# Kernel tuning notes

Measured on AMD Instinct MI355X. Metric: run time of the kernel, lower is better.

Reference implementation:

```python
import jax, jax.numpy as jnp
import numpy as np

B, S, D, H, T_OUT = 256, 256, 64, 1024, 32  # batch, enc seq, input dim, hidden, decode steps


def setup_inputs() -> dict:
    key = jax.random.key(0)
    ks = jax.random.split(key, 15)
    p = lambda k, shape: jax.random.normal(k, shape, jnp.float32) * 0.05
    return {
        "X": jax.random.normal(ks[0], (B, S, D), jnp.float32),
        # encoder LSTM (2 layers); bias = b_ih + b_hh fused (same math)
        "enc_Wih0": p(ks[1], (4 * H, D)), "enc_Whh0": p(ks[2], (4 * H, H)), "enc_b0": p(ks[3], (4 * H,)),
        "enc_Wih1": p(ks[4], (4 * H, H)), "enc_Whh1": p(ks[5], (4 * H, H)), "enc_b1": p(ks[6], (4 * H,)),
        # decoder LSTM (2 layers, scalar input)
        "dec_Wih0": p(ks[7], (4 * H, 1)), "dec_Whh0": p(ks[8], (4 * H, H)), "dec_b0": p(ks[9], (4 * H,)),
        "dec_Wih1": p(ks[10], (4 * H, H)), "dec_Whh1": p(ks[11], (4 * H, H)), "dec_b1": p(ks[12], (4 * H,)),
        # output projection hidden -> 1
        "fc_W": p(ks[13], (1, H)), "fc_b": p(ks[14], (1,)),
    }


def _cell(x, h, c, Wih, Whh, b):
    # torch LSTM cell, gate order i, f, g, o
    gates = x @ Wih.T + h @ Whh.T + b  # [B, 4H]
    i, f, g, o = jnp.split(gates, 4, axis=-1)
    c = jax.nn.sigmoid(f) * c + jax.nn.sigmoid(i) * jnp.tanh(g)
    h = jax.nn.sigmoid(o) * jnp.tanh(c)
    return h, c


def reference(X, enc_Wih0, enc_Whh0, enc_b0, enc_Wih1, enc_Whh1, enc_b1,
              dec_Wih0, dec_Whh0, dec_b0, dec_Wih1, dec_Whh1, dec_b1,
              fc_W, fc_b):
    batch = X.shape[0]
    zeros = jnp.zeros((batch, H), X.dtype)

    def enc_layer(Wih, Whh, b, xs):  # xs: [S, B, Din]
        def step(carry, x_t):
            h, c = carry
            h, c = _cell(x_t, h, c, Wih, Whh, b)
            return (h, c), h
        (h, c), hs = jax.lax.scan(step, (zeros, zeros), xs)
        return hs, h, c

    xs = jnp.swapaxes(X, 0, 1)  # time-major [S, B, D]
    hs0, h0, c0 = enc_layer(enc_Wih0, enc_Whh0, enc_b0, xs)
    _, h1, c1 = enc_layer(enc_Wih1, enc_Whh1, enc_b1, hs0)

    inp0 = jnp.zeros((batch, 1), X.dtype)

    def dec_step(carry, _):
        dh0, dc0, dh1, dc1, inp = carry
        dh0, dc0 = _cell(inp, dh0, dc0, dec_Wih0, dec_Whh0, dec_b0)
        dh1, dc1 = _cell(dh0, dh1, dc1, dec_Wih1, dec_Whh1, dec_b1)
        pred = dh1 @ fc_W.T + fc_b  # [B, 1]; dropout is identity at inference
        return (dh0, dc0, dh1, dc1, pred), pred

    _, preds = jax.lax.scan(dec_step, (h0, c0, h1, c1, inp0), None, length=T_OUT)
    return jnp.transpose(preds, (1, 0, 2))  # [B, T_OUT, 1]
```

## Files before the change

### kernel.cpp

```cpp
#include <hip/hip_runtime.h>

#define B_ 256
#define S_ 256
#define D_ 64
#define H_ 1024
#define G4 4096
#define TOUT 32

typedef unsigned short u16;
typedef __attribute__((ext_vector_type(8))) short short8;
typedef __attribute__((ext_vector_type(4))) float float4v;

__device__ __forceinline__ float bf2f(u16 b) {
  return __uint_as_float(((unsigned int)b) << 16);
}
__device__ __forceinline__ u16 f2bf(float f) {
  unsigned int u = __float_as_uint(f);
  unsigned int r = (u + 0x7fffu + ((u >> 16) & 1u)) >> 16;
  return (u16)r;
}
__device__ __forceinline__ unsigned pack2(float a, float b) {
  return (unsigned)f2bf(a) | ((unsigned)f2bf(b) << 16);
}
__device__ __forceinline__ float sigm(float x) {
  return 1.f / (1.f + __expf(-x));
}
__device__ __forceinline__ float tanh_(float x) {
  float xc = fminf(fmaxf(x, -15.f), 15.f);
  float e = __expf(2.f * xc);
  return (e - 1.f) / (e + 1.f);
}

__global__ __launch_bounds__(256) void cvt_kernel(const float* __restrict__ src,
                                                  u16* __restrict__ dst, int n) {
  for (int i = blockIdx.x * blockDim.x + threadIdx.x; i < n;
       i += gridDim.x * blockDim.x)
    dst[i] = f2bf(src[i]);
}

__global__ __launch_bounds__(256) void zero_kernel(uint4* __restrict__ p, int n16) {
  for (int i = blockIdx.x * blockDim.x + threadIdx.x; i < n16;
       i += gridDim.x * blockDim.x)
    p[i] = make_uint4(0u, 0u, 0u, 0u);
}

struct LayerDesc {
  const u16* A0; int lda0;
  const u16* A1; int lda1; int klen0;
  const void* W0; int ldw0;
  const void* W1; int ldw1; int Ktot;
  const float* bias;
  const float* wcol;
  const float* inp;
  float* c;
  u16* h;
  int active;
  float* gout;
  const float* fcW;
  float* pred;
};

template <bool WF32>
__global__ __launch_bounds__(256) void lstm_step_kernel(LayerDesc dA, LayerDesc dB)
{
  const bool second = (blockIdx.y >= 4);
  const LayerDesc d = second ? dB : dA;
  if (!d.active) return;

  __shared__ u16 As[2][64][72];
  __shared__ u16 Bs[2][64][72];
  __shared__ float Gs[64][68];

  const int tid = threadIdx.x;
  const int m0 = (second ? (blockIdx.y - 4) : blockIdx.y) * 64;
  const int n0 = blockIdx.x * 64;
  const int ub = n0 >> 2;
  const int r = tid >> 2;
  const int q = tid & 3;
  const int lane = tid & 63;
  const int wv = tid >> 6;
  const int wm = (wv >> 1) * 32;
  const int wn = (wv & 1) * 32;
  const int l16 = lane & 15;
  const int quad = lane >> 4;

  const int klen0 = d.klen0;
  const u16* aw0 = d.A0 + (size_t)(m0 + r) * d.lda0;
  const u16* aw1 = d.A1 + (size_t)(m0 + r) * d.lda1;
  const int orow = (r & 3) * H_ + ub + (r >> 2);
  const u16* bw0_h = (const u16*)d.W0 + (size_t)orow * d.ldw0;
  const u16* bw1_h = (const u16*)d.W1 + (size_t)orow * d.ldw1;
  const float* bw0_f = (const float*)d.W0 + (size_t)orow * d.ldw0;
  const float* bw1_f = (const float*)d.W1 + (size_t)orow * d.ldw1;

  uint4 av0, av1, bv0, bv1;
  float4 bf0, bf1, bf2, bf3;

  auto load_chunk = [&](int kc) {
    const int kg = kc * 64 + q * 16;
    const bool first = kg < klen0;
    const u16* pa = first ? (aw0 + kg) : (aw1 + (kg - klen0));
    av0 = *(const uint4*)pa;
    av1 = *(const uint4*)(pa + 8);
    if constexpr (WF32) {
      const float* pb = first ? (bw0_f + kg) : (bw1_f + (kg - klen0));
      bf0 = *(const float4*)pb;
      bf1 = *(const float4*)(pb + 4);
      bf2 = *(const float4*)(pb + 8);
      bf3 = *(const float4*)(pb + 12);
    } else {
      const u16* pb = first ? (bw0_h + kg) : (bw1_h + (kg - klen0));
      bv0 = *(const uint4*)pb;
      bv1 = *(const uint4*)(pb + 8);
    }
  };

  auto stage = [&](int buf) {
    if constexpr (WF32) {
      bv0 = make_uint4(pack2(bf0.x, bf0.y), pack2(bf0.z, bf0.w),
                       pack2(bf1.x, bf1.y), pack2(bf1.z, bf1.w));
      bv1 = make_uint4(pack2(bf2.x, bf2.y), pack2(bf2.z, bf2.w),
                       pack2(bf3.x, bf3.y), pack2(bf3.z, bf3.w));
    }
    *(uint4*)&As[buf][r][q * 16]     = av0;
    *(uint4*)&As[buf][r][q * 16 + 8] = av1;
    *(uint4*)&Bs[buf][r][q * 16]     = bv0;
    *(uint4*)&Bs[buf][r][q * 16 + 8] = bv1;
  };

  float4v acc00 = {}, acc01 = {}, acc10 = {}, acc11 = {};
  const int nch = d.Ktot >> 6;

  load_chunk(0);
  stage(0);
  if (nch > 1) load_chunk(1);
  __syncthreads();

  for (int kc = 0; kc < nch; ++kc) {
    const int cur = kc & 1;
#pragma unroll
    for (int ks = 0; ks < 2; ++ks) {
      const int kb = ks * 32 + quad * 8;
      short8 a0 = *(const short8*)&As[cur][wm + l16][kb];
      short8 a1 = *(const short8*)&As[cur][wm + 16 + l16][kb];
      short8 b0 = *(const short8*)&Bs[cur][wn + l16][kb];
      short8 b1 = *(const short8*)&Bs[cur][wn + 16 + l16][kb];
      acc00 = __builtin_amdgcn_mfma_f32_16x16x32_bf16(a0, b0, acc00, 0, 0, 0);
      acc01 = __builtin_amdgcn_mfma_f32_16x16x32_bf16(a0, b1, acc01, 0, 0, 0);
      acc10 = __builtin_amdgcn_mfma_f32_16x16x32_bf16(a1, b0, acc10, 0, 0, 0);
      acc11 = __builtin_amdgcn_mfma_f32_16x16x32_bf16(a1, b1, acc11, 0, 0, 0);
    }
    if (kc + 1 < nch) {
      stage(cur ^ 1);
      if (kc + 2 < nch) load_chunk(kc + 2);
      __syncthreads();
    }
  }

#pragma unroll
  for (int rr = 0; rr < 4; ++rr) {
    Gs[wm + quad * 4 + rr][wn + l16]           = acc00[rr];
    Gs[wm + quad * 4 + rr][wn + 16 + l16]      = acc01[rr];
    Gs[wm + 16 + quad * 4 + rr][wn + l16]      = acc10[rr];
    Gs[wm + 16 + quad * 4 + rr][wn + 16 + l16] = acc11[rr];
  }
  __syncthreads();

  if (d.gout != nullptr) {
#pragma unroll
    for (int it = 0; it < 4; ++it) {
      const int p = tid + it * 256;
      const int bl = p >> 4;
      const int u = p & 15;
      const int J = ub + u;
      const int bg = m0 + bl;
      const float4v g = *(const float4v*)&Gs[bl][u * 4];
      *(float4*)&d.gout[((size_t)bg * H_ + J) * 4] =
          make_float4(g[0], g[1], g[2], g[3]);
    }
    return;
  }

#pragma unroll
  for (int it = 0; it < 4; ++it) {
    const int p = tid + it * 256;
    const int bl = p >> 4;
    const int u = p & 15;
    const int J = ub + u;
    const int bg = m0 + bl;
    const float4v g = *(const float4v*)&Gs[bl][u * 4];
    float pi = g[0] + d.bias[J];
    float pf = g[1] + d.bias[H_ + J];
    float pg = g[2] + d.bias[2 * H_ + J];
    float po = g[3] + d.bias[3 * H_ + J];
    if (d.inp != nullptr) {
      const float iv = d.inp[bg];
      pi += iv * d.wcol[J];
      pf += iv * d.wcol[H_ + J];
      pg += iv * d.wcol[2 * H_ + J];
      po += iv * d.wcol[3 * H_ + J];
    }
    const size_t idx = (size_t)bg * H_ + J;
    const float c = d.c[idx];
    const float cn = sigm(pf) * c + sigm(pi) * tanh_(pg);
    d.c[idx] = cn;
    const float hv = sigm(po) * tanh_(cn);
    d.h[idx] = f2bf(hv);
    if (d.pred != nullptr) {
      float s = hv * d.fcW[J];
      s += __shfl_xor(s, 1, 64);
      s += __shfl_xor(s, 2, 64);
      s += __shfl_xor(s, 4, 64);
      s += __shfl_xor(s, 8, 64);
      if (u == 0) atomicAdd(&d.pred[bg], s);
    }
  }
}

__global__ __launch_bounds__(256) void dec_cell_kernel(
    const float* __restrict__ GBUF, const float* __restrict__ bias,
    const float* __restrict__ wcol, const float* __restrict__ pred_prev,
    const float* __restrict__ fcb, float* __restrict__ C,
    u16* __restrict__ hout)
{
  const int b = blockIdx.x;
  const int tid = threadIdx.x;
  const float iv = (pred_prev != nullptr) ? (pred_prev[b] + fcb[0]) : 0.f;
#pragma unroll
  for (int k = 0; k < 4; ++k) {
    const int J = tid + k * 256;
    const float4 g = *(const float4*)&GBUF[((size_t)b * H_ + J) * 4];
    const float pi = g.x + bias[J]          + iv * wcol[J];
    const float pf = g.y + bias[H_ + J]     + iv * wcol[H_ + J];
    const float pg = g.z + bias[2 * H_ + J] + iv * wcol[2 * H_ + J];
    const float po = g.w + bias[3 * H_ + J] + iv * wcol[3 * H_ + J];
    const size_t idx = (size_t)b * H_ + J;
    const float c0 = C[idx];
    const float cn = sigm(pf) * c0 + sigm(pi) * tanh_(pg);
    C[idx] = cn;
    hout[idx] = f2bf(sigm(po) * tanh_(cn));
  }
}

__global__ __launch_bounds__(256) void dec_out_kernel(
    const float* __restrict__ PRED, const float* __restrict__ fcb,
    float* __restrict__ out)
{
  const int gid = blockIdx.x * 256 + threadIdx.x;
  const int b = gid >> 5;
  const int t = gid & 31;
  out[gid] = PRED[t * B_ + b] + fcb[0];
}

__global__ __launch_bounds__(256) void fc_kernel(
    const u16* __restrict__ h1, const float* __restrict__ fcW,
    const float* __restrict__ fcb, float* __restrict__ out,
    float* __restrict__ inp, int t)
{
  const int b = blockIdx.x;
  const int tid = threadIdx.x;
  const u16* hr = h1 + (size_t)b * H_ + tid * 4;
  const float* wr = fcW + tid * 4;
  float s = 0.f;
#pragma unroll
  for (int j = 0; j < 4; ++j) s += bf2f(hr[j]) * wr[j];
#pragma unroll
  for (int off = 32; off > 0; off >>= 1) s += __shfl_down(s, off, 64);
  __shared__ float red[4];
  if ((tid & 63) == 0) red[tid >> 6] = s;
  __syncthreads();
  if (tid == 0) {
    const float p = red[0] + red[1] + red[2] + red[3] + fcb[0];
    out[(size_t)b * TOUT + t] = p;
    inp[b] = p;
  }
}

extern "C" void kernel_launch(void* const* d_in, const int* in_sizes, int n_in,
                              void* d_out, int out_size, void* d_ws, size_t ws_size,
                              hipStream_t stream)
{
  const float* X     = (const float*)d_in[0];
  const float* eWih0 = (const float*)d_in[1];
  const float* eWhh0 = (const float*)d_in[2];
  const float* eb0   = (const float*)d_in[3];
  const float* eWih1 = (const float*)d_in[4];
  const float* eWhh1 = (const float*)d_in[5];
  const float* eb1   = (const float*)d_in[6];
  const float* dWih0 = (const float*)d_in[7];
  const float* dWhh0 = (const float*)d_in[8];
  const float* db0   = (const float*)d_in[9];
  const float* dWih1 = (const float*)d_in[10];
  const float* dWhh1 = (const float*)d_in[11];
  const float* db1   = (const float*)d_in[12];
  const float* fcW   = (const float*)d_in[13];
  const float* fcb   = (const float*)d_in[14];
  float* out = (float*)d_out;

  char* ws = (char*)d_ws;
  size_t off = 0;
  auto alloc = [&](size_t bytes) -> void* {
    void* p = ws + off;
    off += (bytes + 255) & ~(size_t)255;
    return p;
  };
  u16* h0buf[2], *h1buf[2];
  h0buf[0] = (u16*)alloc((size_t)B_ * H_ * 2);
  h0buf[1] = (u16*)alloc((size_t)B_ * H_ * 2);
  h1buf[0] = (u16*)alloc((size_t)B_ * H_ * 2);
  h1buf[1] = (u16*)alloc((size_t)B_ * H_ * 2);
  float* C0   = (float*)alloc((size_t)B_ * H_ * 4);
  float* C1   = (float*)alloc((size_t)B_ * H_ * 4);
  float* INP  = (float*)alloc(B_ * 4);
  float* PRED = (float*)alloc((size_t)TOUT * B_ * 4);
  const size_t zbytes = off;
  u16* XB = (u16*)alloc((size_t)B_ * S_ * D_ * 2);
  u16* WB_eWih0 = (u16*)alloc((size_t)G4 * D_ * 2);
  u16* WB_eWhh0 = (u16*)alloc((size_t)G4 * H_ * 2);
  u16* WB_eWih1 = (u16*)alloc((size_t)G4 * H_ * 2);
  u16* WB_eWhh1 = (u16*)alloc((size_t)G4 * H_ * 2);
  u16* WB_dWhh0 = (u16*)alloc((size_t)G4 * H_ * 2);
  u16* WB_dWih1 = (u16*)alloc((size_t)G4 * H_ * 2);
  u16* WB_dWhh1 = (u16*)alloc((size_t)G4 * H_ * 2);
  float* GBUF   = (float*)alloc((size_t)B_ * H_ * 4 * 4);
  const size_t need_full = off;
  const bool fast = (ws_size >= need_full);

  zero_kernel<<<dim3(256), dim3(256), 0, stream>>>((uint4*)ws, (int)(zbytes / 16));
  cvt_kernel<<<dim3(1024), dim3(256), 0, stream>>>(X, XB, B_ * S_ * D_);
  if (fast) {
    cvt_kernel<<<dim3(256), dim3(256), 0, stream>>>(eWih0, WB_eWih0, G4 * D_);
    cvt_kernel<<<dim3(1024), dim3(256), 0, stream>>>(eWhh0, WB_eWhh0, G4 * H_);
    cvt_kernel<<<dim3(1024), dim3(256), 0, stream>>>(eWih1, WB_eWih1, G4 * H_);
    cvt_kernel<<<dim3(1024), dim3(256), 0, stream>>>(eWhh1, WB_eWhh1, G4 * H_);
    cvt_kernel<<<dim3(1024), dim3(256), 0, stream>>>(dWhh0, WB_dWhh0, G4 * H_);
    cvt_kernel<<<dim3(1024), dim3(256), 0, stream>>>(dWih1, WB_dWih1, G4 * H_);
    cvt_kernel<<<dim3(1024), dim3(256), 0, stream>>>(dWhh1, WB_dWhh1, G4 * H_);
  }

  auto mk = [&](const u16* A0, int lda0, const u16* A1, int lda1, int klen0,
                const void* W0b, const void* W0f, int ldw0,
                const void* W1b, const void* W1f, int ldw1, int Ktot,
                const float* bias, const float* wcol, const float* inp,
                float* c, u16* h) {
    LayerDesc d;
    d.A0 = A0; d.lda0 = lda0; d.A1 = A1; d.lda1 = lda1; d.klen0 = klen0;
    d.W0 = fast ? W0b : W0f; d.ldw0 = ldw0;
    d.W1 = fast ? W1b : W1f; d.ldw1 = ldw1; d.Ktot = Ktot;
    d.bias = bias; d.wcol = wcol; d.inp = inp; d.c = c; d.h = h;
    d.active = 1;
    d.gout = nullptr; d.fcW = nullptr; d.pred = nullptr;
    return d;
  };
  LayerDesc off_d = {};
  off_d.active = 0;

  auto launch = [&](dim3 grid, const LayerDesc& a, const LayerDesc& b) {
    if (fast)
      lstm_step_kernel<false><<<grid, dim3(256), 0, stream>>>(a, b);
    else
      lstm_step_kernel<true><<<grid, dim3(256), 0, stream>>>(a, b);
  };

  for (int u = 0; u <= S_; ++u) {
    LayerDesc d0 = off_d, d1 = off_d;
    if (u < S_) {
      const int t = u;
      d0 = mk(XB + t * D_, S_ * D_, h0buf[t & 1], H_, D_,
              WB_eWih0, eWih0, D_, WB_eWhh0, eWhh0, H_, 1088,
              eb0, nullptr, nullptr, C0, h0buf[(t + 1) & 1]);
    }
    if (u >= 1) {
      const int t = u - 1;
      d1 = mk(h0buf[(t + 1) & 1], H_, h1buf[t & 1], H_, H_,
              WB_eWih1, eWih1, H_, WB_eWhh1, eWhh1, H_, 2048,
              eb1, nullptr, nullptr, C1, h1buf[(t + 1) & 1]);
    }
    launch(dim3(64, 8), d0, d1);
  }

  if (fast) {
    LayerDesc g0 = mk(h0buf[0], H_, h0buf[0], H_, 1024,
                      WB_dWhh0, dWhh0, H_, WB_dWhh0, dWhh0, H_, 1024,
                      db0, nullptr, nullptr, C0, nullptr);
    g0.gout = GBUF;
    launch(dim3(64, 4), g0, off_d);
    dec_cell_kernel<<<dim3(B_), dim3(256), 0, stream>>>(
        GBUF, db0, dWih0, nullptr, fcb, C0, h0buf[1]);

    for (int t = 0; t < TOUT; ++t) {
      LayerDesc dA = mk(h0buf[(t + 1) & 1], H_, h1buf[t & 1], H_, 1024,
                        WB_dWih1, dWih1, H_, WB_dWhh1, dWhh1, H_, 2048,
                        db1, nullptr, nullptr, C1, h1buf[(t + 1) & 1]);
      dA.fcW = fcW;
      dA.pred = PRED + (size_t)t * B_;
      LayerDesc dB = off_d;
      const bool more = (t + 1 < TOUT);
      if (more) {
        dB = mk(h0buf[(t + 1) & 1], H_, h0buf[(t + 1) & 1], H_, 1024,
                WB_dWhh0, dWhh0, H_, WB_dWhh0, dWhh0, H_, 1024,
                db0, nullptr, nullptr, C0, nullptr);
        dB.gout = GBUF;
      }
      launch(dim3(64, more ? 8 : 4), dA, dB);
      if (more)
        dec_cell_kernel<<<dim3(B_), dim3(256), 0, stream>>>(
            GBUF, db0, dWih0, PRED + (size_t)t * B_, fcb, C0, h0buf[t & 1]);
    }
    dec_out_kernel<<<dim3(TOUT), dim3(256), 0, stream>>>(PRED, fcb, out);
    return;
  }

  for (int t = 0; t < TOUT; ++t) {
    u16* h0i = h0buf[t & 1]; u16* h0o = h0buf[(t + 1) & 1];
    u16* h1i = h1buf[t & 1]; u16* h1o = h1buf[(t + 1) & 1];
    LayerDesc dl0 = mk(h0i, H_, h0i, H_, 1024,
                       WB_dWhh0, dWhh0, H_, WB_dWhh0, dWhh0, H_, 1024,
                       db0, dWih0, INP, C0, h0o);
    launch(dim3(64, 4), dl0, off_d);
    LayerDesc dl1 = mk(h0o, H_, h1i, H_, H_,
                       WB_dWih1, dWih1, H_, WB_dWhh1, dWhh1, H_, 2048,
                       db1, nullptr, nullptr, C1, h1o);
    launch(dim3(64, 4), dl1, off_d);
    fc_kernel<<<dim3(B_), dim3(256), 0, stream>>>(h1o, fcW, fcb, out, INP, t);
  }
}
```

Baseline: 6.142 ms.

## Switch LSTM step GEMM to 32x32 MFMA with split-K across waves

```diff
diff --git a/kernel.cpp b/kernel.cpp
--- a/kernel.cpp
+++ b/kernel.cpp
@@ -10,6 +10,7 @@
 typedef unsigned short u16;
 typedef __attribute__((ext_vector_type(8))) short short8;
 typedef __attribute__((ext_vector_type(4))) float float4v;
+typedef __attribute__((ext_vector_type(16))) float f32x16;
 
 __device__ __forceinline__ float bf2f(u16 b) {
   return __uint_as_float(((unsigned int)b) << 16);
@@ -67,9 +68,11 @@
   const LayerDesc d = second ? dB : dA;
   if (!d.active) return;
 
-  __shared__ u16 As[2][64][72];
-  __shared__ u16 Bs[2][64][72];
-  __shared__ float Gs[64][68];
+  __shared__ __align__(16) unsigned char SMEM[54272];
+  u16 (*As)[64][72] = (u16(*)[64][72])(SMEM);
+  u16 (*Bs)[64][72] = (u16(*)[64][72])(SMEM + 18432);
+  float* Gs = (float*)(SMEM + 36864);
+  float* scr = (float*)SMEM;
 
   const int tid = threadIdx.x;
   const int m0 = (second ? (blockIdx.y - 4) : blockIdx.y) * 64;
@@ -79,10 +82,8 @@
   const int q = tid & 3;
   const int lane = tid & 63;
   const int wv = tid >> 6;
-  const int wm = (wv >> 1) * 32;
-  const int wn = (wv & 1) * 32;
+  const int l31 = lane & 31;
   const int l16 = lane & 15;
-  const int quad = lane >> 4;
 
   const int klen0 = d.klen0;
   const u16* aw0 = d.A0 + (size_t)(m0 + r) * d.lda0;
@@ -128,7 +129,8 @@
     *(uint4*)&Bs[buf][r][q * 16 + 8] = bv1;
   };
 
-  float4v acc00 = {}, acc01 = {}, acc10 = {}, acc11 = {};
+  f32x16 acc00 = {}, acc01 = {}, acc10 = {}, acc11 = {};
+  const int kb = wv * 16 + (lane >> 5) * 8;
   const int nch = d.Ktot >> 6;
 
   load_chunk(0);
@@ -138,18 +140,14 @@
 
   for (int kc = 0; kc < nch; ++kc) {
     const int cur = kc & 1;
-#pragma unroll
-    for (int ks = 0; ks < 2; ++ks) {
-      const int kb = ks * 32 + quad * 8;
-      short8 a0 = *(const short8*)&As[cur][wm + l16][kb];
-      short8 a1 = *(const short8*)&As[cur][wm + 16 + l16][kb];
-      short8 b0 = *(const short8*)&Bs[cur][wn + l16][kb];
-      short8 b1 = *(const short8*)&Bs[cur][wn + 16 + l16][kb];
-      acc00 = __builtin_amdgcn_mfma_f32_16x16x32_bf16(a0, b0, acc00, 0, 0, 0);
-      acc01 = __builtin_amdgcn_mfma_f32_16x16x32_bf16(a0, b1, acc01, 0, 0, 0);
-      acc10 = __builtin_amdgcn_mfma_f32_16x16x32_bf16(a1, b0, acc10, 0, 0, 0);
-      acc11 = __builtin_amdgcn_mfma_f32_16x16x32_bf16(a1, b1, acc11, 0, 0, 0);
-    }
+    const short8 a0 = *(const short8*)&As[cur][l31][kb];
+    const short8 a1 = *(const short8*)&As[cur][l31 + 32][kb];
+    const short8 b0 = *(const short8*)&Bs[cur][l31][kb];
+    const short8 b1 = *(const short8*)&Bs[cur][l31 + 32][kb];
+    acc00 = __builtin_amdgcn_mfma_f32_32x32x16_bf16(a0, b0, acc00, 0, 0, 0);
+    acc01 = __builtin_amdgcn_mfma_f32_32x32x16_bf16(a0, b1, acc01, 0, 0, 0);
+    acc10 = __builtin_amdgcn_mfma_f32_32x32x16_bf16(a1, b0, acc10, 0, 0, 0);
+    acc11 = __builtin_amdgcn_mfma_f32_32x32x16_bf16(a1, b1, acc11, 0, 0, 0);
     if (kc + 1 < nch) {
       stage(cur ^ 1);
       if (kc + 2 < nch) load_chunk(kc + 2);
@@ -157,12 +155,46 @@
     }
   }
 
-#pragma unroll
-  for (int rr = 0; rr < 4; ++rr) {
-    Gs[wm + quad * 4 + rr][wn + l16]           = acc00[rr];
-    Gs[wm + quad * 4 + rr][wn + 16 + l16]      = acc01[rr];
-    Gs[wm + 16 + quad * 4 + rr][wn + l16]      = acc10[rr];
-    Gs[wm + 16 + quad * 4 + rr][wn + 16 + l16] = acc11[rr];
+  __syncthreads();
+
+  auto store_frag = [&](const f32x16& A, int qd) {
+    if (qd == wv) return;
+    const int slot = (wv > qd) ? (wv - 1) : wv;
+    float* rg = scr + (qd * 3 + slot) * 1024 + lane * 4;
+#pragma unroll
+    for (int j4 = 0; j4 < 4; ++j4)
+      *(float4*)&rg[j4 * 256] = make_float4(A[j4 * 4 + 0], A[j4 * 4 + 1],
+                                            A[j4 * 4 + 2], A[j4 * 4 + 3]);
+  };
+  store_frag(acc00, 0);
+  store_frag(acc01, 1);
+  store_frag(acc10, 2);
+  store_frag(acc11, 3);
+  __syncthreads();
+
+  f32x16 fin = (wv == 0) ? acc00 : (wv == 1) ? acc01 : (wv == 2) ? acc10 : acc11;
+#pragma unroll
+  for (int s = 0; s < 3; ++s) {
+    const float* rg = scr + (wv * 3 + s) * 1024 + lane * 4;
+#pragma unroll
+    for (int j4 = 0; j4 < 4; ++j4) {
+      const float4 v = *(const float4*)&rg[j4 * 256];
+      fin[j4 * 4 + 0] += v.x;
+      fin[j4 * 4 + 1] += v.y;
+      fin[j4 * 4 + 2] += v.z;
+      fin[j4 * 4 + 3] += v.w;
+    }
+  }
+  __syncthreads();
+
+  {
+    const int rbase = (wv >> 1) * 32 + (lane >> 5) * 4;
+    const int col = (wv & 1) * 32 + l31;
+#pragma unroll
+    for (int j = 0; j < 16; ++j) {
+      const int row = rbase + (j & 3) + 8 * (j >> 2);
+      Gs[row * 68 + col] = fin[j];
+    }
   }
   __syncthreads();
 
@@ -174,7 +206,7 @@
       const int u = p & 15;
       const int J = ub + u;
       const int bg = m0 + bl;
-      const float4v g = *(const float4v*)&Gs[bl][u * 4];
+      const float4v g = *(const float4v*)&Gs[bl * 68 + u * 4];
       *(float4*)&d.gout[((size_t)bg * H_ + J) * 4] =
           make_float4(g[0], g[1], g[2], g[3]);
     }
@@ -188,7 +220,7 @@
     const int u = p & 15;
     const int J = ub + u;
     const int bg = m0 + bl;
-    const float4v g = *(const float4v*)&Gs[bl][u * 4];
+    const float4v g = *(const float4v*)&Gs[bl * 68 + u * 4];
     float pi = g[0] + d.bias[J];
     float pf = g[1] + d.bias[H_ + J];
     float pg = g[2] + d.bias[2 * H_ + J];
```

Result: no change. 6.048 ms (-1.5%).
